# Kernel tuning notes

Hardware: AMD Instinct MI355X
Metric: run time of the kernel (lower is better)

Reference implementation:

```python
import jax, jax.numpy as jnp
import numpy as np

EPS = 1e-5  # BatchNorm eps


def setup_inputs() -> dict:
    key = jax.random.key(0)
    ks = jax.random.split(key, 13)
    B, C, H, W = 8, 256, 64, 64
    Ci = 128
    s = 0.05
    return {
        "x": jax.random.normal(ks[0], (B, C, H, W), jnp.float32),
        "Wt": jax.random.normal(ks[1], (Ci, C), jnp.float32) * s,
        "bt": jax.random.normal(ks[2], (Ci,), jnp.float32) * s,
        "Wp": jax.random.normal(ks[3], (Ci, C), jnp.float32) * s,
        "bp": jax.random.normal(ks[4], (Ci,), jnp.float32) * s,
        "Wg": jax.random.normal(ks[5], (Ci, C), jnp.float32) * s,
        "bg": jax.random.normal(ks[6], (Ci,), jnp.float32) * s,
        "Wz": jax.random.normal(ks[7], (C, Ci), jnp.float32) * s,
        "bz": jax.random.normal(ks[8], (C,), jnp.float32) * s,
        "gamma": jax.random.normal(ks[9], (C,), jnp.float32) * s,
        "beta": jax.random.normal(ks[10], (C,), jnp.float32) * s,
        "rmean": jax.random.normal(ks[11], (C,), jnp.float32) * s,
        "rvar": jax.random.uniform(ks[12], (C,), jnp.float32, 0.5, 1.5),
    }


def reference(x, Wt, bt, Wp, bp, Wg, bg, Wz, bz, gamma, beta, rmean, rvar):
    B, C, H, W = x.shape
    N = H * W
    xf = x.reshape(B, C, N)                                  # [B,C,N]
    # 1x1 conv projections == channel GEMMs
    theta = jnp.einsum('oc,bcn->bno', Wt, xf) + bt           # [B,N,Ci]
    phi = jnp.einsum('oc,bcn->bon', Wp, xf) + bp[:, None]    # [B,Ci,N]
    g = jnp.einsum('oc,bcn->bno', Wg, xf) + bg               # [B,N,Ci]
    # single-head attention over all N=H*W positions
    attn = jax.nn.softmax(jnp.einsum('bnc,bcm->bnm', theta, phi), axis=-1)
    y = jnp.einsum('bnm,bmc->bnc', attn, g)                  # [B,N,Ci]
    # W_z: 1x1 conv + BatchNorm (eval mode: running stats) + residual
    z = jnp.einsum('oc,bnc->bon', Wz, y) + bz[:, None]       # [B,C,N]
    inv = gamma / jnp.sqrt(rvar + EPS)                       # [C]
    zn = (z - rmean[:, None]) * inv[:, None] + beta[:, None]
    return zn.reshape(B, C, H, W) + x
```

## Files before the change

kernel.cpp:

```cpp
#include <hip/hip_runtime.h>
#include <stdint.h>

typedef __attribute__((ext_vector_type(8))) short bf16x8;
typedef __attribute__((ext_vector_type(4))) float f32x4;
typedef __attribute__((ext_vector_type(16))) float f32x16;

__device__ __forceinline__ unsigned short f32_to_bf16(float f) {
  union { float f; uint32_t u; } v; v.f = f;
  uint32_t u = v.u;
  u += 0x7fffu + ((u >> 16) & 1u);
  return (unsigned short)(u >> 16);
}

__device__ __forceinline__ float bf16_to_f32(unsigned short s) {
  union { uint32_t u; float f; } v; v.u = ((uint32_t)s) << 16;
  return v.f;
}

__device__ __forceinline__ uint32_t cvt_pk_bf16(float a, float b) {
  uint32_t r;
  asm("v_cvt_pk_bf16_f32 %0, %1, %2" : "=v"(r) : "v"(a), "v"(b));
  return r;
}

__device__ __forceinline__ void async_copy16(void* lds, const void* g) {
  __builtin_amdgcn_global_load_lds(
      (const __attribute__((address_space(1))) unsigned int*)g,
      (__attribute__((address_space(3))) unsigned int*)lds, 16, 0, 0);
}

__global__ __launch_bounds__(256) void xpose_kernel(
    const float* __restrict__ x, unsigned short* __restrict__ xT,
    unsigned short* __restrict__ xc) {
  __shared__ unsigned short ts[32][260];
  const int t = threadIdx.x;
  const int bid = blockIdx.x;
  const int b = bid >> 7;
  const int ct = (bid >> 4) & 7;
  const int nt = bid & 15;
  const int c0 = ct * 32, n0 = nt * 256;

  const float* xb = x + ((size_t)b * 256 + c0) * 4096 + n0;
#pragma unroll
  for (int i = 0; i < 8; ++i) {
    int flat = i * 256 + t;
    int c = flat >> 6, nq = flat & 63;
    float4 v = *(const float4*)(xb + (size_t)c * 4096 + nq * 4);
    union { uint2 u; unsigned short s[4]; } pk;
    pk.s[0] = f32_to_bf16(v.x); pk.s[1] = f32_to_bf16(v.y);
    pk.s[2] = f32_to_bf16(v.z); pk.s[3] = f32_to_bf16(v.w);
    *(uint2*)&ts[c][nq * 4] = pk.u;
    *(uint2*)(xc + ((size_t)b * 256 + c0 + c) * 4096 + n0 + nq * 4) = pk.u;
  }
  __syncthreads();

  unsigned short* xo = xT + ((size_t)b * 4096 + n0) * 256 + c0;
#pragma unroll
  for (int i = 0; i < 4; ++i) {
    int flat = i * 256 + t;
    int n = flat >> 2, ch = flat & 3;
    union { uint4 u; unsigned short s[8]; } pk;
#pragma unroll
    for (int jj = 0; jj < 8; ++jj) pk.s[jj] = ts[ch * 8 + jj][n];
    *(uint4*)(xo + (size_t)n * 256 + ch * 8) = pk.u;
  }
}

__global__ __launch_bounds__(256) void wcvt_kernel(
    const float* __restrict__ Wt, const float* __restrict__ Wp,
    const float* __restrict__ Wg, const float* __restrict__ Wz,
    unsigned short* __restrict__ Wcat, unsigned short* __restrict__ Wzb) {
  int e = (blockIdx.x * 256 + threadIdx.x) * 4;
  const float* src;
  unsigned short* dst;
  int off;
  if (e < 32768) { src = Wt; dst = Wcat; off = e; }
  else if (e < 65536) { src = Wp; dst = Wcat + 32768; off = e - 32768; }
  else if (e < 98304) { src = Wg; dst = Wcat + 65536; off = e - 65536; }
  else { src = Wz; dst = Wzb; off = e - 98304; }
  float4 v = *(const float4*)(src + off);
  union { uint2 u; unsigned short s[4]; } pk;
  pk.s[0] = f32_to_bf16(v.x); pk.s[1] = f32_to_bf16(v.y);
  pk.s[2] = f32_to_bf16(v.z); pk.s[3] = f32_to_bf16(v.w);
  *(uint2*)(dst + off) = pk.u;
}

__global__ __launch_bounds__(512, 2) void proj_kernel(
    const unsigned short* __restrict__ xT,
    const unsigned short* __restrict__ Wcat,
    const float* __restrict__ bt, const float* __restrict__ bp,
    const float* __restrict__ bg,
    unsigned short* __restrict__ Q, unsigned short* __restrict__ Km,
    unsigned short* __restrict__ Vt) {
  __shared__ __align__(1024) unsigned short xs[128 * 256];
  const int t = threadIdx.x;
  const int lane = t & 63;
  const int w = t >> 6;
  const int nt = blockIdx.x;
  const int b = blockIdx.y;
  const int n0 = nt * 128;

  const unsigned char* xTb =
      (const unsigned char*)(xT + ((size_t)b * 4096 + n0) * 256);
  unsigned char* lbase = (unsigned char*)xs;
#pragma unroll
  for (int i = 0; i < 8; ++i) {
    int base = (w * 8 + i) * 1024;
    int off = base + lane * 16;
    int n = off >> 9;
    int bir = off & 511;
    async_copy16(lbase + base, xTb + n * 512 + (bir ^ ((n & 7) << 4)));
  }
  __syncthreads();

  const int rl = lane & 15, gh = lane >> 4;
  const int swz = (rl & 7) << 4;
  const int rlv = (rl & 3) | ((rl & 4) << 1) | ((rl & 8) >> 1);

  f32x4 aQ[8], aK[8], aV[8];
#pragma unroll
  for (int i = 0; i < 8; ++i) {
    aQ[i] = (f32x4){0.f, 0.f, 0.f, 0.f};
    aK[i] = (f32x4){0.f, 0.f, 0.f, 0.f};
    aV[i] = (f32x4){0.f, 0.f, 0.f, 0.f};
  }

  const unsigned char* wq =
      (const unsigned char*)Wcat + ((w * 16 + rl) * 256) * 2 + gh * 16;
  const unsigned char* wk = wq + 128 * 512;
  const unsigned char* wv = wq + 256 * 512;

#pragma unroll
  for (int kk = 0; kk < 8; ++kk) {
    bf16x8 xf[8];
#pragma unroll
    for (int n2 = 0; n2 < 8; ++n2)
      xf[n2] = *(const bf16x8*)(lbase + (n2 * 16 + rl) * 512 +
                                ((kk * 64 + gh * 16) ^ swz));
    bf16x8 fq = *(const bf16x8*)(wq + kk * 64);
    bf16x8 fk = *(const bf16x8*)(wk + kk * 64);
    bf16x8 fv = *(const bf16x8*)(wv + kk * 64);
#pragma unroll
    for (int n2 = 0; n2 < 8; ++n2) {
      aQ[n2] = __builtin_amdgcn_mfma_f32_16x16x32_bf16(xf[n2], fq, aQ[n2], 0, 0, 0);
      aK[n2] = __builtin_amdgcn_mfma_f32_16x16x32_bf16(xf[n2], fk, aK[n2], 0, 0, 0);
      aV[n2] = __builtin_amdgcn_mfma_f32_16x16x32_bf16(fv, xf[n2], aV[n2], 0, 0, 0);
    }
  }

  const float btv = bt[w * 16 + rl];
  const float bpv = bp[w * 16 + rl];
  float bgv[4];
#pragma unroll
  for (int j = 0; j < 4; ++j) bgv[j] = bg[w * 16 + gh * 4 + j];

  unsigned short* Qb = Q + ((size_t)b * 4096 + n0) * 128 + w * 16 + rl;
  unsigned short* Kb = Km + ((size_t)b * 4096 + n0) * 128 + w * 16 + rl;
  unsigned short* Vb = Vt + (size_t)b * 128 * 4096 + n0 + rlv;
#pragma unroll
  for (int n2 = 0; n2 < 8; ++n2) {
#pragma unroll
    for (int j = 0; j < 4; ++j) {
      int n = n2 * 16 + gh * 4 + j;
      Qb[(size_t)n * 128] = f32_to_bf16(aQ[n2][j] + btv);
      Kb[(size_t)n * 128] = f32_to_bf16(aK[n2][j] + bpv);
      int o = w * 16 + gh * 4 + j;
      Vb[(size_t)o * 4096 + n2 * 16] = f32_to_bf16(aV[n2][j] + bgv[j]);
    }
  }
}

__global__ __launch_bounds__(256, 2) void attn_kernel(
    const unsigned short* __restrict__ Qg,
    const unsigned short* __restrict__ Kg,
    const unsigned short* __restrict__ Vg,
    unsigned short* __restrict__ Opart,
    float* __restrict__ Marr, float* __restrict__ Larr) {
  __shared__ __align__(1024) unsigned char smem[65536];
  const int t = threadIdx.x;
  const int lane = t & 63;
  const int w = t >> 6;
  const int q31 = lane & 31;
  const int hi = lane >> 5;
  const int kswz = (q31 & 15) << 4;

  const int orig = blockIdx.x;
  const int b = orig & 7;
  const int idx = orig >> 3;
  const int h = idx & 1;
  const int qg = idx >> 1;
  const int qw = qg * 128 + w * 32;
  const int kv0 = h * 2048;

  const unsigned short* Qb = Qg + (size_t)b * 4096 * 128;
  const unsigned short* Kb = Kg + (size_t)b * 4096 * 128;
  const unsigned short* Vb = Vg + (size_t)b * 128 * 4096;

  bf16x8 qf[8];
  {
    const unsigned char* qp =
        (const unsigned char*)(Qb + (size_t)(qw + q31) * 128) + hi * 16;
#pragma unroll
    for (int dc = 0; dc < 8; ++dc) qf[dc] = *(const bf16x8*)(qp + dc * 32);
  }

  const unsigned char* ksrc[4];
  const unsigned char* vsrc[4];
  unsigned int kofs[4], vofs[4];
#pragma unroll
  for (int ii = 0; ii < 4; ++ii) {
    int seg = w * 4 + ii;
    {
      int r = seg * 4 + (lane >> 4);
      int kcol = ((lane & 15) * 16) ^ ((r & 15) << 4);
      ksrc[ii] = (const unsigned char*)(Kb + (size_t)(kv0 + r) * 128) + kcol;
      kofs[ii] = seg * 1024;
    }
    {
      int o = seg * 1024 + lane * 16;
      int R = o >> 8;
      int cp = (o & 255) ^ ((R & 15) << 4);
      int d = 2 * R + (cp >> 7);
      int kvb = cp & 127;
      vsrc[ii] = (const unsigned char*)(Vb + (size_t)d * 4096 + kv0) + kvb;
      vofs[ii] = 16384 + seg * 1024;
    }
  }

  f32x16 acc[4];
#pragma unroll
  for (int i = 0; i < 4; ++i)
#pragma unroll
    for (int e = 0; e < 16; ++e) acc[i][e] = 0.f;
  float m = -1e30f, l = 0.f;

#pragma unroll
  for (int ii = 0; ii < 4; ++ii) {
    async_copy16(smem + kofs[ii], ksrc[ii]);
    async_copy16(smem + vofs[ii], vsrc[ii]);
  }
  __syncthreads();

#pragma unroll 2
  for (int it = 0; it < 32; ++it) {
    unsigned char* bb = smem + (it & 1) * 32768;
    if (it + 1 < 32) {
      unsigned int nb = ((it + 1) & 1) * 32768;
      size_t ko = (size_t)(it + 1) * 16384;
      int vo2 = (it + 1) * 128;
#pragma unroll
      for (int ii = 0; ii < 4; ++ii) {
        async_copy16(smem + nb + kofs[ii], ksrc[ii] + ko);
        async_copy16(smem + nb + vofs[ii], vsrc[ii] + vo2);
      }
    }

    f32x16 st0, st1;
#pragma unroll
    for (int e = 0; e < 16; ++e) { st0[e] = 0.f; st1[e] = 0.f; }
    const unsigned char* kb0 = bb + q31 * 256;
    const unsigned char* kb1 = bb + (32 + q31) * 256;
    __builtin_amdgcn_s_setprio(1);
#pragma unroll
    for (int dc = 0; dc < 8; ++dc) {
      int off = (dc * 32 + hi * 16) ^ kswz;
      bf16x8 k0 = *(const bf16x8*)(kb0 + off);
      bf16x8 k1 = *(const bf16x8*)(kb1 + off);
      st0 = __builtin_amdgcn_mfma_f32_32x32x16_bf16(k0, qf[dc], st0, 0, 0, 0);
      st1 = __builtin_amdgcn_mfma_f32_32x32x16_bf16(k1, qf[dc], st1, 0, 0, 0);
    }
    __builtin_amdgcn_s_setprio(0);

    float tmax = st0[0];
#pragma unroll
    for (int e = 1; e < 16; ++e) tmax = fmaxf(tmax, st0[e]);
#pragma unroll
    for (int e = 0; e < 16; ++e) tmax = fmaxf(tmax, st1[e]);
#pragma unroll
    for (int off = 1; off < 64; off <<= 1)
      tmax = fmaxf(tmax, __shfl_xor(tmax, off));
    if (tmax > m + 8.f) {
      float mn = fmaxf(m, tmax);
      float sc = __expf(m - mn);
      m = mn;
      l *= sc;
#pragma unroll
      for (int i = 0; i < 4; ++i)
#pragma unroll
        for (int e = 0; e < 16; ++e) acc[i][e] *= sc;
    }
    float ls = 0.f;
#pragma unroll
    for (int e = 0; e < 16; ++e) { st0[e] = __expf(st0[e] - m); ls += st0[e]; }
#pragma unroll
    for (int e = 0; e < 16; ++e) { st1[e] = __expf(st1[e] - m); ls += st1[e]; }
    l += ls;

    const unsigned char* vbase = bb + 16384 + (q31 >> 1) * 256;
    const int vhb = (q31 & 1) << 7;
    const int vswz = (q31 >> 1) << 4;
#pragma unroll
    for (int ks = 0; ks < 4; ++ks) {
      union { uint32_t u[4]; bf16x8 v; } pk;
      if (ks == 0) {
        pk.u[0] = cvt_pk_bf16(st0[0], st0[1]);
        pk.u[1] = cvt_pk_bf16(st0[2], st0[3]);
        pk.u[2] = cvt_pk_bf16(st0[4], st0[5]);
        pk.u[3] = cvt_pk_bf16(st0[6], st0[7]);
      } else if (ks == 1) {
        pk.u[0] = cvt_pk_bf16(st0[8], st0[9]);
        pk.u[1] = cvt_pk_bf16(st0[10], st0[11]);
        pk.u[2] = cvt_pk_bf16(st0[12], st0[13]);
        pk.u[3] = cvt_pk_bf16(st0[14], st0[15]);
      } else if (ks == 2) {
        pk.u[0] = cvt_pk_bf16(st1[0], st1[1]);
        pk.u[1] = cvt_pk_bf16(st1[2], st1[3]);
        pk.u[2] = cvt_pk_bf16(st1[4], st1[5]);
        pk.u[3] = cvt_pk_bf16(st1[6], st1[7]);
      } else {
        pk.u[0] = cvt_pk_bf16(st1[8], st1[9]);
        pk.u[1] = cvt_pk_bf16(st1[10], st1[11]);
        pk.u[2] = cvt_pk_bf16(st1[12], st1[13]);
        pk.u[3] = cvt_pk_bf16(st1[14], st1[15]);
      }
      __builtin_amdgcn_s_setprio(1);
#pragma unroll
      for (int dt = 0; dt < 4; ++dt) {
        bf16x8 vf = *(const bf16x8*)(
            vbase + dt * 4096 + ((vhb | (ks * 32 + hi * 16)) ^ vswz));
        acc[dt] = __builtin_amdgcn_mfma_f32_32x32x16_bf16(pk.v, vf, acc[dt], 0, 0, 0);
      }
      __builtin_amdgcn_s_setprio(0);
    }
    __syncthreads();
  }

  float lf = l + __shfl_xor(l, 32);
  if (lane < 32) {
    size_t ix = (size_t)h * 32768 + (size_t)b * 4096 + qw + q31;
    Marr[ix] = m;
    Larr[ix] = lf;
  }
  unsigned short* ob = Opart + (size_t)h * 32768 * 128;
#pragma unroll
  for (int dt = 0; dt < 4; ++dt)
#pragma unroll
    for (int r = 0; r < 16; ++r) {
      int qrow = qw + (r & 3) + 8 * (r >> 2) + 4 * hi;
      ob[((size_t)b * 4096 + qrow) * 128 + dt * 32 + q31] =
          f32_to_bf16(acc[dt][r]);
    }
}

__global__ __launch_bounds__(512, 2) void outz_kernel(
    const unsigned short* __restrict__ Opart,
    const float* __restrict__ Marr, const float* __restrict__ Larr,
    const unsigned short* __restrict__ Wzb,
    const unsigned short* __restrict__ xc, const float* __restrict__ bz,
    const float* __restrict__ gamma, const float* __restrict__ beta,
    const float* __restrict__ rmean, const float* __restrict__ rvar,
    float* __restrict__ out) {
  __shared__ __align__(1024) unsigned short ys[128 * 128];
  const int t = threadIdx.x;
  const int lane = t & 63;
  const int w = t >> 6;
  const int nt = blockIdx.x;
  const int b = blockIdx.y;
  const int n0 = nt * 128;

  unsigned char* lbase = (unsigned char*)ys;
#pragma unroll
  for (int i = 0; i < 4; ++i) {
    int off = (w * 4 + i) * 1024 + lane * 16;
    int n = off >> 8;
    int cb = (off & 255) ^ ((n & 7) << 4);
    size_t qidx = (size_t)b * 4096 + n0 + n;
    float m0 = Marr[qidx], m1 = Marr[32768 + qidx];
    float l0 = Larr[qidx], l1 = Larr[32768 + qidx];
    float M = fmaxf(m0, m1);
    float e0 = __expf(m0 - M), e1 = __expf(m1 - M);
    float rd = 1.f / (e0 * l0 + e1 * l1);
    float f0 = e0 * rd, f1 = e1 * rd;
    const unsigned char* ob = (const unsigned char*)Opart;
    const bf16x8 o0 = *(const bf16x8*)(ob + qidx * 256 + cb);
    const bf16x8 o1 = *(const bf16x8*)(ob + 32768ull * 256 + qidx * 256 + cb);
    union { uint4 u4; unsigned short s[8]; } pk;
#pragma unroll
    for (int e = 0; e < 8; ++e)
      pk.s[e] = f32_to_bf16(f0 * bf16_to_f32((unsigned short)o0[e]) +
                            f1 * bf16_to_f32((unsigned short)o1[e]));
    *(uint4*)(lbase + off) = pk.u4;
  }
  __syncthreads();

  const int rl = lane & 15, gh = lane >> 4;
  const int swz = (rl & 7) << 4;

  f32x4 acc[2][8];
#pragma unroll
  for (int i = 0; i < 2; ++i)
#pragma unroll
    for (int j = 0; j < 8; ++j) acc[i][j] = (f32x4){0.f, 0.f, 0.f, 0.f};

  const unsigned char* wz0 =
      (const unsigned char*)Wzb + ((w * 2) * 16 + rl) * 256 + gh * 16;

#pragma unroll
  for (int kk = 0; kk < 4; ++kk) {
    bf16x8 yf[8];
#pragma unroll
    for (int n2 = 0; n2 < 8; ++n2)
      yf[n2] = *(const bf16x8*)(lbase + (n2 * 16 + rl) * 256 +
                                ((kk * 64 + gh * 16) ^ swz));
    bf16x8 f0 = *(const bf16x8*)(wz0 + kk * 64);
    bf16x8 f1 = *(const bf16x8*)(wz0 + 16 * 256 + kk * 64);
#pragma unroll
    for (int n2 = 0; n2 < 8; ++n2) {
      acc[0][n2] = __builtin_amdgcn_mfma_f32_16x16x32_bf16(f0, yf[n2], acc[0][n2], 0, 0, 0);
      acc[1][n2] = __builtin_amdgcn_mfma_f32_16x16x32_bf16(f1, yf[n2], acc[1][n2], 0, 0, 0);
    }
  }

#pragma unroll
  for (int ot = 0; ot < 2; ++ot) {
#pragma unroll
    for (int j = 0; j < 4; ++j) {
      int o = (w * 2 + ot) * 16 + gh * 4 + j;
      float scale = gamma[o] * rsqrtf(rvar[o] + 1e-5f);
      float shift = (bz[o] - rmean[o]) * scale + beta[o];
      const unsigned short* xr = xc + ((size_t)b * 256 + o) * 4096 + n0;
      float* orow = out + ((size_t)b * 256 + o) * 4096 + n0;
#pragma unroll
      for (int n2 = 0; n2 < 8; ++n2) {
        int n = n2 * 16 + rl;
        orow[n] = acc[ot][n2][j] * scale + shift + bf16_to_f32(xr[n]);
      }
    }
  }
}

extern "C" void kernel_launch(void* const* d_in, const int* in_sizes, int n_in,
                              void* d_out, int out_size, void* d_ws,
                              size_t ws_size, hipStream_t stream) {
  const float* x     = (const float*)d_in[0];
  const float* Wt    = (const float*)d_in[1];
  const float* bt    = (const float*)d_in[2];
  const float* Wp    = (const float*)d_in[3];
  const float* bp    = (const float*)d_in[4];
  const float* Wg    = (const float*)d_in[5];
  const float* bg    = (const float*)d_in[6];
  const float* Wz    = (const float*)d_in[7];
  const float* bz    = (const float*)d_in[8];
  const float* gamma = (const float*)d_in[9];
  const float* beta  = (const float*)d_in[10];
  const float* rmean = (const float*)d_in[11];
  const float* rvar  = (const float*)d_in[12];
  float* out = (float*)d_out;

  const size_t NE = (size_t)8 * 4096 * 128;
  unsigned short* Wcat  = (unsigned short*)d_ws;
  unsigned short* Wzb   = Wcat + 98304;
  float*          Marr  = (float*)(Wzb + 32768);
  float*          Larr  = Marr + 2 * 32768;
  unsigned short* xT    = (unsigned short*)(Larr + 2 * 32768);
  unsigned short* Q     = xT + 2 * NE;
  unsigned short* Km    = Q + NE;
  unsigned short* Vt    = Km + NE;
  unsigned short* xc    = Vt + NE;
  unsigned short* Opart = xT;

  wcvt_kernel<<<128, 256, 0, stream>>>(Wt, Wp, Wg, Wz, Wcat, Wzb);
  xpose_kernel<<<1024, 256, 0, stream>>>(x, xT, xc);
  proj_kernel<<<dim3(32, 8), 512, 0, stream>>>(xT, Wcat, bt, bp, bg, Q, Km, Vt);
  attn_kernel<<<512, 256, 0, stream>>>(Q, Km, Vt, Opart, Marr, Larr);
  outz_kernel<<<dim3(32, 8), 512, 0, stream>>>(Opart, Marr, Larr, Wzb, xc, bz,
                                               gamma, beta, rmean, rvar, out);
}
```

Measured before the change: 130.5 us.

## Fuse x transpose/bf16 conversion into projection kernel and read fp32 residual directly

Removes the separate transpose kernel. The projection kernel now loads fp32 x directly, converts it to bf16, and transposes it through a small LDS staging tile into the swizzled layout the MFMA loop expects. The output kernel reads the fp32 x residual instead of a bf16 copy, which also improves residual precision. This saves one launch and a round trip of intermediate buffers through global memory, at the cost of a serialized, synchronized load loop in the projection kernel that gives up the earlier async LDS copy.

```diff
diff --git a/kernel.cpp b/kernel.cpp
--- a/kernel.cpp
+++ b/kernel.cpp
@@ -27,43 +27,6 @@
   __builtin_amdgcn_global_load_lds(
       (const __attribute__((address_space(1))) unsigned int*)g,
       (__attribute__((address_space(3))) unsigned int*)lds, 16, 0, 0);
-}
-
-__global__ __launch_bounds__(256) void xpose_kernel(
-    const float* __restrict__ x, unsigned short* __restrict__ xT,
-    unsigned short* __restrict__ xc) {
-  __shared__ unsigned short ts[32][260];
-  const int t = threadIdx.x;
-  const int bid = blockIdx.x;
-  const int b = bid >> 7;
-  const int ct = (bid >> 4) & 7;
-  const int nt = bid & 15;
-  const int c0 = ct * 32, n0 = nt * 256;
-
-  const float* xb = x + ((size_t)b * 256 + c0) * 4096 + n0;
-#pragma unroll
-  for (int i = 0; i < 8; ++i) {
-    int flat = i * 256 + t;
-    int c = flat >> 6, nq = flat & 63;
-    float4 v = *(const float4*)(xb + (size_t)c * 4096 + nq * 4);
-    union { uint2 u; unsigned short s[4]; } pk;
-    pk.s[0] = f32_to_bf16(v.x); pk.s[1] = f32_to_bf16(v.y);
-    pk.s[2] = f32_to_bf16(v.z); pk.s[3] = f32_to_bf16(v.w);
-    *(uint2*)&ts[c][nq * 4] = pk.u;
-    *(uint2*)(xc + ((size_t)b * 256 + c0 + c) * 4096 + n0 + nq * 4) = pk.u;
-  }
-  __syncthreads();
-
-  unsigned short* xo = xT + ((size_t)b * 4096 + n0) * 256 + c0;
-#pragma unroll
-  for (int i = 0; i < 4; ++i) {
-    int flat = i * 256 + t;
-    int n = flat >> 2, ch = flat & 3;
-    union { uint4 u; unsigned short s[8]; } pk;
-#pragma unroll
-    for (int jj = 0; jj < 8; ++jj) pk.s[jj] = ts[ch * 8 + jj][n];
-    *(uint4*)(xo + (size_t)n * 256 + ch * 8) = pk.u;
-  }
 }
 
 __global__ __launch_bounds__(256) void wcvt_kernel(
@@ -86,13 +49,14 @@
 }
 
 __global__ __launch_bounds__(512, 2) void proj_kernel(
-    const unsigned short* __restrict__ xT,
+    const float* __restrict__ x,
     const unsigned short* __restrict__ Wcat,
     const float* __restrict__ bt, const float* __restrict__ bp,
     const float* __restrict__ bg,
     unsigned short* __restrict__ Q, unsigned short* __restrict__ Km,
     unsigned short* __restrict__ Vt) {
   __shared__ __align__(1024) unsigned short xs[128 * 256];
+  __shared__ unsigned short tmp[32][132];
   const int t = threadIdx.x;
   const int lane = t & 63;
   const int w = t >> 6;
@@ -100,18 +64,33 @@
   const int b = blockIdx.y;
   const int n0 = nt * 128;
 
-  const unsigned char* xTb =
-      (const unsigned char*)(xT + ((size_t)b * 4096 + n0) * 256);
+  const float* xb = x + (size_t)b * 256 * 4096;
   unsigned char* lbase = (unsigned char*)xs;
-#pragma unroll
-  for (int i = 0; i < 8; ++i) {
-    int base = (w * 8 + i) * 1024;
-    int off = base + lane * 16;
-    int n = off >> 9;
-    int bir = off & 511;
-    async_copy16(lbase + base, xTb + n * 512 + (bir ^ ((n & 7) << 4)));
-  }
-  __syncthreads();
+
+  for (int cc = 0; cc < 8; ++cc) {
+#pragma unroll
+    for (int i = 0; i < 2; ++i) {
+      int idx = i * 512 + t;
+      int c = idx >> 5;
+      int n4 = (idx & 31) * 4;
+      float4 v = *(const float4*)(xb + (size_t)(cc * 32 + c) * 4096 + n0 + n4);
+      union { uint2 u; unsigned short s[4]; } pk;
+      pk.s[0] = f32_to_bf16(v.x); pk.s[1] = f32_to_bf16(v.y);
+      pk.s[2] = f32_to_bf16(v.z); pk.s[3] = f32_to_bf16(v.w);
+      *(uint2*)&tmp[c][n4] = pk.u;
+    }
+    __syncthreads();
+    {
+      int n = t >> 2;
+      int ch = t & 3;
+      union { uint4 u; unsigned short s[8]; } pk;
+#pragma unroll
+      for (int jj = 0; jj < 8; ++jj) pk.s[jj] = tmp[ch * 8 + jj][n];
+      int byt = n * 512 + ((cc * 64 + ch * 16) ^ ((n & 7) << 4));
+      *(uint4*)(lbase + byt) = pk.u;
+    }
+    __syncthreads();
+  }
 
   const int rl = lane & 15, gh = lane >> 4;
   const int swz = (rl & 7) << 4;
@@ -356,7 +335,7 @@
     const unsigned short* __restrict__ Opart,
     const float* __restrict__ Marr, const float* __restrict__ Larr,
     const unsigned short* __restrict__ Wzb,
-    const unsigned short* __restrict__ xc, const float* __restrict__ bz,
+    const float* __restrict__ x, const float* __restrict__ bz,
     const float* __restrict__ gamma, const float* __restrict__ beta,
     const float* __restrict__ rmean, const float* __restrict__ rvar,
     float* __restrict__ out) {
@@ -428,12 +407,12 @@
       int o = (w * 2 + ot) * 16 + gh * 4 + j;
       float scale = gamma[o] * rsqrtf(rvar[o] + 1e-5f);
       float shift = (bz[o] - rmean[o]) * scale + beta[o];
-      const unsigned short* xr = xc + ((size_t)b * 256 + o) * 4096 + n0;
+      const float* xr = x + ((size_t)b * 256 + o) * 4096 + n0;
       float* orow = out + ((size_t)b * 256 + o) * 4096 + n0;
 #pragma unroll
       for (int n2 = 0; n2 < 8; ++n2) {
         int n = n2 * 16 + rl;
-        orow[n] = acc[ot][n2][j] * scale + shift + bf16_to_f32(xr[n]);
+        orow[n] = acc[ot][n2][j] * scale + shift + xr[n];
       }
     }
   }
@@ -462,17 +441,14 @@
   unsigned short* Wzb   = Wcat + 98304;
   float*          Marr  = (float*)(Wzb + 32768);
   float*          Larr  = Marr + 2 * 32768;
-  unsigned short* xT    = (unsigned short*)(Larr + 2 * 32768);
-  unsigned short* Q     = xT + 2 * NE;
+  unsigned short* Opart = (unsigned short*)(Larr + 2 * 32768);
+  unsigned short* Q     = Opart + 2 * NE;
   unsigned short* Km    = Q + NE;
   unsigned short* Vt    = Km + NE;
-  unsigned short* xc    = Vt + NE;
-  unsigned short* Opart = xT;
 
   wcvt_kernel<<<128, 256, 0, stream>>>(Wt, Wp, Wg, Wz, Wcat, Wzb);
-  xpose_kernel<<<1024, 256, 0, stream>>>(x, xT, xc);
-  proj_kernel<<<dim3(32, 8), 512, 0, stream>>>(xT, Wcat, bt, bp, bg, Q, Km, Vt);
+  proj_kernel<<<dim3(32, 8), 512, 0, stream>>>(x, Wcat, bt, bp, bg, Q, Km, Vt);
   attn_kernel<<<512, 256, 0, stream>>>(Q, Km, Vt, Opart, Marr, Larr);
-  outz_kernel<<<dim3(32, 8), 512, 0, stream>>>(Opart, Marr, Larr, Wzb, xc, bz,
+  outz_kernel<<<dim3(32, 8), 512, 0, stream>>>(Opart, Marr, Larr, Wzb, x, bz,
                                                gamma, beta, rmean, rvar, out);
 }
```

New measurement: 125.3 us. 1.04x faster.
